# Kernel tuning notes

Measured on AMD Instinct MI355X. Metric: run time of the kernel, lower is better.

Reference implementation:

```python
import jax, jax.numpy as jnp
import numpy as np

B, N, H, W, C = 512, 16, 84, 84, 3
CNN_OUT, ATTN, GH, HEADS, POS, A_DIM = 256, 64, 128, 2, 3, 3
IN_GAT = CNN_OUT + POS  # 259
FLAT = 64 * 16 * 16     # conv output flat dim for 84x84 input


def setup_inputs() -> dict:
    key = jax.random.key(0)
    ks = jax.random.split(key, 16)
    s = 0.05
    return dict(
        cam=jax.random.uniform(ks[0], (B, H, W, C), jnp.float32),
        pos=jax.random.normal(ks[1], (B, POS), jnp.float32),
        team_pos=jax.random.normal(ks[2], (B, N, POS), jnp.float32) * 10.0,
        agent_idx=jax.random.randint(ks[3], (B,), 0, N),
        W1=jax.random.normal(ks[4], (32, C, 8, 8), jnp.float32) * s, b1=jnp.zeros((32,), jnp.float32),
        W2=jax.random.normal(ks[5], (64, 32, 4, 4), jnp.float32) * s, b2=jnp.zeros((64,), jnp.float32),
        W3=jax.random.normal(ks[6], (64, 64, 3, 3), jnp.float32) * s, b3=jnp.zeros((64,), jnp.float32),
        Wp=jax.random.normal(ks[7], (FLAT, CNN_OUT), jnp.float32) * 0.01, bp=jnp.zeros((CNN_OUT,), jnp.float32),
        Wid=jax.random.normal(ks[8], (1, ATTN), jnp.float32) * s, bid=jnp.zeros((ATTN,), jnp.float32),
        Wg=jax.random.normal(ks[9], (IN_GAT, HEADS * GH), jnp.float32) * s,
        a_src=jax.random.normal(ks[10], (HEADS, GH), jnp.float32) * s,
        a_dst=jax.random.normal(ks[11], (HEADS, GH), jnp.float32) * s,
        Wh1=jax.random.normal(ks[12], (HEADS * GH + ATTN, 256), jnp.float32) * s, bh1=jnp.zeros((256,), jnp.float32),
        Wh2=jax.random.normal(ks[13], (256, 2 * A_DIM), jnp.float32) * s, bh2=jnp.zeros((2 * A_DIM,), jnp.float32),
    )


def _conv(x, w, b, stride):
    y = jax.lax.conv_general_dilated(x, w, (stride, stride), 'VALID',
                                     dimension_numbers=('NCHW', 'OIHW', 'NCHW'))
    return jax.nn.relu(y + b[None, :, None, None])


def reference(cam, pos, team_pos, agent_idx, W1, b1, W2, b2, W3, b3, Wp, bp,
              Wid, bid, Wg, a_src, a_dst, Wh1, bh1, Wh2, bh2):
    # CNN encoder (NHWC -> NCHW)
    x = jnp.transpose(cam, (0, 3, 1, 2))
    x = _conv(x, W1, b1, 2)   # [B,32,39,39]
    x = _conv(x, W2, b2, 2)   # [B,64,18,18]
    x = _conv(x, W3, b3, 1)   # [B,64,16,16]
    cam_feat = jax.nn.relu(x.reshape(x.shape[0], -1) @ Wp + bp)  # [B,256]

    # per-node features: broadcast ego cam feat + relative team positions
    rel_pos = team_pos - pos[:, None, :]                                     # [B,N,3]
    node_feats = jnp.concatenate(
        [jnp.broadcast_to(cam_feat[:, None, :], (B, N, CNN_OUT)), rel_pos], axis=-1)  # [B,N,259]

    # adjacency: within 100m, no self-loops, self-loop added for isolated nodes
    dist = jnp.linalg.norm(team_pos[:, :, None, :] - team_pos[:, None, :, :], axis=-1)  # [B,N,N]
    eye = jnp.eye(N, dtype=node_feats.dtype)
    adj = (dist < 100.0).astype(node_feats.dtype) * (1.0 - eye)
    need_self = (adj.sum(axis=2) == 0).astype(adj.dtype)                     # [B,N]
    adj = adj + eye[None] * need_self[..., None]

    # dense multi-head GAT layer
    hN = (node_feats @ Wg).reshape(B, N, HEADS, GH)                          # [B,N,H,D]
    src = jnp.einsum('bnhd,hd->bnh', hN, a_src)
    dst = jnp.einsum('bnhd,hd->bnh', hN, a_dst)
    e = jax.nn.leaky_relu(src[:, :, None, :] + dst[:, None, :, :], 0.2)      # [B,i,j,H]
    e = jnp.where(adj[..., None] > 0, e, -1e9)
    alpha = jax.nn.softmax(e, axis=2)
    h = jnp.einsum('bijh,bjhd->bihd', alpha, hN).reshape(B, N, HEADS * GH)   # [B,N,256]
    h = jax.nn.elu(h)
    h = jnp.nan_to_num(h, nan=0.0, posinf=0.0, neginf=0.0)

    # agent-id embedding, fuse, gather own node, policy head
    id_emb = jax.nn.relu(agent_idx.astype(jnp.float32)[:, None] @ Wid + bid)  # [B,64]
    fused = jnp.concatenate([h, jnp.broadcast_to(id_emb[:, None, :], (B, N, ATTN))], axis=-1)  # [B,N,320]
    agent_feat = fused[jnp.arange(B), agent_idx]                             # [B,320]
    z = jax.nn.relu(agent_feat @ Wh1 + bh1)
    logits = z @ Wh2 + bh2                                                    # [B,6]
    return logits
```

## Files before the change

kernel.cpp:

```cpp
#include <hip/hip_runtime.h>


typedef __attribute__((ext_vector_type(8))) short bf16x8;
typedef __attribute__((ext_vector_type(4))) float f32x4;

union U4 { uint4 v; unsigned int u[4]; bf16x8 h; };

__device__ __forceinline__ unsigned short f2bf(float x) {
    unsigned int u = __float_as_uint(x);
    return (unsigned short)((u + 0x7FFFu + ((u >> 16) & 1u)) >> 16);
}
__device__ __forceinline__ unsigned int pack2(float lo, float hi) {
    return (unsigned int)f2bf(lo) | ((unsigned int)f2bf(hi) << 16);
}
__device__ __forceinline__ bf16x8 loadA(const unsigned int* __restrict__ W, int k8, int M, int oc) {
    U4 r; r.v = *(const uint4*)(W + (((size_t)k8 * M + oc) << 2));
    return r.h;
}
__device__ __forceinline__ bf16x8 loadB4(const unsigned int* __restrict__ base, size_t idx) {
    U4 r; r.v = *(const uint4*)(base + (idx << 2));
    return r.h;
}
#define MFMA(a, b, c) __builtin_amdgcn_mfma_f32_16x16x32_bf16((a), (b), (c), 0, 0, 0)

__device__ __forceinline__ int xcd_swz(int L, int nwg) {
    int q = nwg >> 3, r = nwg & 7;
    int x = L & 7, i = L >> 3;
    return (x < r ? x * (q + 1) : r * (q + 1) + (x - r) * q) + i;
}

__device__ __forceinline__ void storeK(unsigned int* __restrict__ out,
                                       size_t row, size_t BC, size_t bcol,
                                       int lg, unsigned int u0, unsigned int u1) {
    uint2 v; v.x = u0; v.y = u1;
    *(uint2*)(out + ((row * BC + bcol) << 2) + ((lg & 1) << 1)) = v;
}

__global__ __launch_bounds__(256) void prepack(
    const float* __restrict__ W1, const float* __restrict__ W2,
    const float* __restrict__ W3, const float* __restrict__ Wp,
    const float* __restrict__ Wg, const float* __restrict__ Wh1,
    unsigned int* __restrict__ W1t, unsigned int* __restrict__ W2t,
    unsigned int* __restrict__ W3t, unsigned int* __restrict__ Wpt,
    unsigned int* __restrict__ Wgt, unsigned int* __restrict__ Wh1t)
{
    int i = blockIdx.x * 256 + threadIdx.x;
    if (i < 4096) {
        int j2 = i & 3, oc = (i >> 2) & 31, k8 = i >> 7;
        int kh = k8 >> 2, kwp = k8 & 3;
        float w[2];
        #pragma unroll
        for (int e = 0; e < 2; e++) {
            int jj = 2 * j2 + e;
            int kwlo = jj >> 2, c = jj & 3;
            w[e] = (c == 3) ? 0.f
                 : W1[((oc * 3 + c) * 8 + kh) * 8 + 2 * kwp + kwlo];
        }
        W1t[i] = pack2(w[0], w[1]);
    } else if (i < 20480) {
        int j = i - 4096;
        int j2 = j & 3, oc = (j >> 2) & 63, k8 = j >> 8;
        int tap = k8 >> 2, ic = (k8 & 3) * 8 + 2 * j2;
        int kh = tap >> 2, kw = tap & 3;
        float a = W2[((oc * 32 + ic) * 4 + kh) * 4 + kw];
        float b = W2[((oc * 32 + ic + 1) * 4 + kh) * 4 + kw];
        W2t[j] = pack2(a, b);
    } else if (i < 38912) {
        int j = i - 20480;
        int j2 = j & 3, oc = (j >> 2) & 63, k8 = j >> 8;
        int tap = k8 >> 3, ic = (k8 & 7) * 8 + 2 * j2;
        int kh = tap / 3, kw = tap % 3;
        float a = W3[((oc * 64 + ic) * 3 + kh) * 3 + kw];
        float b = W3[((oc * 64 + ic + 1) * 3 + kh) * 3 + kw];
        W3t[j] = pack2(a, b);
    } else if (i < 2136064) {
        int j = i - 38912;
        int j2 = j & 3, n = (j >> 2) & 255, k8 = j >> 10;
        int s3 = k8 >> 3, oc = (k8 & 7) * 8 + 2 * j2;
        float a = Wp[(size_t)(oc * 256 + s3) * 256 + n];
        float b = Wp[(size_t)((oc + 1) * 256 + s3) * 256 + n];
        Wpt[j] = pack2(a, b);
    } else if (i < 2168832) {
        int j = i - 2136064;
        int j2 = j & 3, m = (j >> 2) & 255, k8 = j >> 10;
        int k = k8 * 8 + 2 * j2;
        Wgt[j] = pack2(Wg[k * 256 + m], Wg[(k + 1) * 256 + m]);
    } else if (i < 2209792) {
        int j = i - 2168832;
        int j2 = j & 3, m = (j >> 2) & 255, k8 = j >> 10;
        int k = k8 * 8 + 2 * j2;
        Wh1t[j] = pack2(Wh1[k * 256 + m], Wh1[(k + 1) * 256 + m]);
    }
}

__global__ __launch_bounds__(256) void transpose_cam(
    const float* __restrict__ cam, unsigned int* __restrict__ camq, int b0, int BC)
{
    __shared__ float lds[32][253];
    int yy = blockIdx.x;
    int bb = blockIdx.y * 32;
    int t = threadIdx.x;
    for (int f = t; f < 8064; f += 256) {
        int b = f / 252, p = f - b * 252;
        lds[b][p] = cam[(size_t)(b0 + bb + b) * 21168 + yy * 252 + p];
    }
    __syncthreads();
    for (int g = t; g < 1344; g += 256) {
        int b = g & 31, xp = g >> 5;
        const float* l = &lds[b][6 * xp];
        uint4 u;
        u.x = pack2(l[0], l[1]);
        u.y = pack2(l[2], 0.f);
        u.z = pack2(l[3], l[4]);
        u.w = pack2(l[5], 0.f);
        *(uint4*)(camq + (((size_t)(yy * 42 + xp) * BC + bb + b) << 2)) = u;
    }
}

__global__ __launch_bounds__(256) void conv1_mfma(
    const unsigned int* __restrict__ in32, const unsigned int* __restrict__ Wt,
    const float* __restrict__ bias, unsigned int* __restrict__ out32,
    int BC, int nspat)
{
    int wgid = xcd_swz(blockIdx.x, gridDim.x);
    int s = wgid % nspat;
    int bq = wgid / nspat;
    int oh = s / 39, ow = s - oh * 39;
    int wv = threadIdx.x >> 6, l = threadIdx.x & 63;
    int lg = l >> 4, lc = l & 15;
    const size_t sBC = (size_t)BC;
    size_t base = (size_t)bq * 256 + wv * 64 + lc;
    f32x4 acc[2][4] = {};
    #pragma unroll
    for (int step = 0; step < 8; step++) {
        bf16x8 A[2], B[4];
        A[0] = loadA(Wt, step * 4 + lg, 32, lc);
        A[1] = loadA(Wt, step * 4 + lg, 32, 16 + lc);
        size_t row = (size_t)((2 * oh + step) * 42 + ow + lg);
        #pragma unroll
        for (int g = 0; g < 4; g++)
            B[g] = loadB4(in32, row * sBC + base + g * 16);
        #pragma unroll
        for (int m = 0; m < 2; m++)
            #pragma unroll
            for (int g = 0; g < 4; g++)
                acc[m][g] = MFMA(A[m], B[g], acc[m][g]);
    }
    #pragma unroll
    for (int m = 0; m < 2; m++) {
        float4 bv = *(const float4*)(bias + m * 16 + lg * 4);
        size_t row = (size_t)s * 4 + 2 * m + (lg >> 1);
        #pragma unroll
        for (int g = 0; g < 4; g++) {
            f32x4 a = acc[m][g];
            unsigned int u0 = pack2(fmaxf(a.x + bv.x, 0.f), fmaxf(a.y + bv.y, 0.f));
            unsigned int u1 = pack2(fmaxf(a.z + bv.z, 0.f), fmaxf(a.w + bv.w, 0.f));
            storeK(out32, row, sBC, base + g * 16, lg, u0, u1);
        }
    }
}

__global__ __launch_bounds__(256) void conv2_mfma(
    const unsigned int* __restrict__ in32, const unsigned int* __restrict__ Wt,
    const float* __restrict__ bias, unsigned int* __restrict__ out32,
    int BC, int nspat)
{
    int wgid = xcd_swz(blockIdx.x, gridDim.x);
    int s = wgid % nspat;
    int bq = wgid / nspat;
    int oh = s / 18, ow = s - oh * 18;
    int wv = threadIdx.x >> 6, l = threadIdx.x & 63;
    int lg = l >> 4, lc = l & 15;
    const size_t sBC = (size_t)BC;
    size_t base = (size_t)bq * 256 + wv * 64 + lc;
    f32x4 acc[4][4] = {};
    int ybase = 2 * oh, xbase = 2 * ow;
    #pragma unroll
    for (int sp = 0; sp < 8; sp++) {
        const int s0 = 2 * sp, s1 = s0 + 1;
        bf16x8 A0[4], A1[4], B0[4], B1[4];
        #pragma unroll
        for (int m = 0; m < 4; m++) {
            A0[m] = loadA(Wt, s0 * 4 + lg, 64, m * 16 + lc);
            A1[m] = loadA(Wt, s1 * 4 + lg, 64, m * 16 + lc);
        }
        {
            const int kh = s0 >> 2, kw = s0 & 3;
            size_t row = (size_t)(((ybase + kh) * 39 + xbase + kw) * 4 + lg);
            #pragma unroll
            for (int g = 0; g < 4; g++)
                B0[g] = loadB4(in32, row * sBC + base + g * 16);
        }
        {
            const int kh = s1 >> 2, kw = s1 & 3;
            size_t row = (size_t)(((ybase + kh) * 39 + xbase + kw) * 4 + lg);
            #pragma unroll
            for (int g = 0; g < 4; g++)
                B1[g] = loadB4(in32, row * sBC + base + g * 16);
        }
        #pragma unroll
        for (int m = 0; m < 4; m++)
            #pragma unroll
            for (int g = 0; g < 4; g++)
                acc[m][g] = MFMA(A0[m], B0[g], acc[m][g]);
        #pragma unroll
        for (int m = 0; m < 4; m++)
            #pragma unroll
            for (int g = 0; g < 4; g++)
                acc[m][g] = MFMA(A1[m], B1[g], acc[m][g]);
    }
    #pragma unroll
    for (int m = 0; m < 4; m++) {
        float4 bv = *(const float4*)(bias + m * 16 + lg * 4);
        size_t row = (size_t)s * 8 + 2 * m + (lg >> 1);
        #pragma unroll
        for (int g = 0; g < 4; g++) {
            f32x4 a = acc[m][g];
            unsigned int u0 = pack2(fmaxf(a.x + bv.x, 0.f), fmaxf(a.y + bv.y, 0.f));
            unsigned int u1 = pack2(fmaxf(a.z + bv.z, 0.f), fmaxf(a.w + bv.w, 0.f));
            storeK(out32, row, sBC, base + g * 16, lg, u0, u1);
        }
    }
}

__global__ __launch_bounds__(256) void conv3_mfma(
    const unsigned int* __restrict__ in32, const unsigned int* __restrict__ Wt,
    const float* __restrict__ bias, unsigned int* __restrict__ out32,
    int BC, int nspat)
{
    int wgid = xcd_swz(blockIdx.x, gridDim.x);
    int s = wgid % nspat;
    int bq = wgid / nspat;
    int oh = s >> 4, ow = s & 15;
    int wv = threadIdx.x >> 6, l = threadIdx.x & 63;
    int lg = l >> 4, lc = l & 15;
    const size_t sBC = (size_t)BC;
    size_t base = (size_t)bq * 256 + wv * 64 + lc;
    f32x4 acc[4][4] = {};
    #pragma unroll
    for (int sp = 0; sp < 9; sp++) {
        const int s0 = 2 * sp, s1 = s0 + 1;
        const int kh = sp / 3, kw = sp - kh * 3;
        bf16x8 A0[4], A1[4], B0[4], B1[4];
        #pragma unroll
        for (int m = 0; m < 4; m++) {
            A0[m] = loadA(Wt, s0 * 4 + lg, 64, m * 16 + lc);
            A1[m] = loadA(Wt, s1 * 4 + lg, 64, m * 16 + lc);
        }
        size_t row0 = (size_t)(((oh + kh) * 18 + ow + kw) * 8 + lg);
        #pragma unroll
        for (int g = 0; g < 4; g++) {
            B0[g] = loadB4(in32, row0 * sBC + base + g * 16);
            B1[g] = loadB4(in32, (row0 + 4) * sBC + base + g * 16);
        }
        #pragma unroll
        for (int m = 0; m < 4; m++)
            #pragma unroll
            for (int g = 0; g < 4; g++)
                acc[m][g] = MFMA(A0[m], B0[g], acc[m][g]);
        #pragma unroll
        for (int m = 0; m < 4; m++)
            #pragma unroll
            for (int g = 0; g < 4; g++)
                acc[m][g] = MFMA(A1[m], B1[g], acc[m][g]);
    }
    #pragma unroll
    for (int m = 0; m < 4; m++) {
        float4 bv = *(const float4*)(bias + m * 16 + lg * 4);
        size_t row = (size_t)s * 8 + 2 * m + (lg >> 1);
        #pragma unroll
        for (int g = 0; g < 4; g++) {
            f32x4 a = acc[m][g];
            unsigned int u0 = pack2(fmaxf(a.x + bv.x, 0.f), fmaxf(a.y + bv.y, 0.f));
            unsigned int u1 = pack2(fmaxf(a.z + bv.z, 0.f), fmaxf(a.w + bv.w, 0.f));
            storeK(out32, row, sBC, base + g * 16, lg, u0, u1);
        }
    }
}

__global__ __launch_bounds__(256) void proj_mfma(
    const unsigned int* __restrict__ x3, const unsigned int* __restrict__ Wpt,
    float* __restrict__ partial, int BC)
{
    int wgid = xcd_swz(blockIdx.x, gridDim.x);
    int rem = wgid & 127;
    int bq = wgid >> 7;
    int mq = rem & 3;
    int kseg = rem >> 2;
    int wv = threadIdx.x >> 6, l = threadIdx.x & 63;
    int lg = l >> 4, lc = l & 15;
    const size_t sBC = (size_t)BC;
    size_t base = (size_t)bq * 256 + wv * 64 + lc;
    f32x4 acc[4][4] = {};
    #pragma unroll
    for (int sp = 0; sp < 8; sp++) {
        const int k8b = kseg * 64 + sp * 8;
        bf16x8 A0[4], A1[4], B0[4], B1[4];
        #pragma unroll
        for (int m = 0; m < 4; m++) {
            A0[m] = loadA(Wpt, k8b + lg, 256, mq * 64 + m * 16 + lc);
            A1[m] = loadA(Wpt, k8b + 4 + lg, 256, mq * 64 + m * 16 + lc);
        }
        #pragma unroll
        for (int g = 0; g < 4; g++) {
            B0[g] = loadB4(x3, (size_t)(k8b + lg) * sBC + base + g * 16);
            B1[g] = loadB4(x3, (size_t)(k8b + 4 + lg) * sBC + base + g * 16);
        }
        #pragma unroll
        for (int m = 0; m < 4; m++)
            #pragma unroll
            for (int g = 0; g < 4; g++)
                acc[m][g] = MFMA(A0[m], B0[g], acc[m][g]);
        #pragma unroll
        for (int m = 0; m < 4; m++)
            #pragma unroll
            for (int g = 0; g < 4; g++)
                acc[m][g] = MFMA(A1[m], B1[g], acc[m][g]);
    }
    #pragma unroll
    for (int m = 0; m < 4; m++) {
        size_t row4 = (size_t)kseg * 64 + mq * 16 + m * 4 + lg;
        #pragma unroll
        for (int g = 0; g < 4; g++)
            *(f32x4*)(partial + ((row4 * sBC + base + g * 16) << 2)) = acc[m][g];
    }
}

__global__ __launch_bounds__(256) void reduce_k(
    const float* __restrict__ partial, const float* __restrict__ bp,
    unsigned int* __restrict__ cf16, int b0, int BC, int bcShift)
{
    int i = blockIdx.x * 256 + threadIdx.x;
    int bl = i & (BC - 1);
    int k8 = i >> bcShift;
    f32x4 S0 = {}, S1 = {};
    for (int seg = 0; seg < 32; seg++) {
        const float* p = partial + (((size_t)(seg * 64 + k8 * 2) * BC + bl) << 2);
        S0 += *(const f32x4*)p;
        S1 += *(const f32x4*)(p + (BC << 2));
    }
    int n = k8 * 8;
    uint4 u;
    u.x = pack2(fmaxf(S0.x + bp[n + 0], 0.f), fmaxf(S0.y + bp[n + 1], 0.f));
    u.y = pack2(fmaxf(S0.z + bp[n + 2], 0.f), fmaxf(S0.w + bp[n + 3], 0.f));
    u.z = pack2(fmaxf(S1.x + bp[n + 4], 0.f), fmaxf(S1.y + bp[n + 5], 0.f));
    u.w = pack2(fmaxf(S1.z + bp[n + 6], 0.f), fmaxf(S1.w + bp[n + 7], 0.f));
    *(uint4*)(cf16 + (((size_t)k8 * 512 + b0 + bl) << 2)) = u;
}

__global__ __launch_bounds__(64) void gat_prep(
    const unsigned int* __restrict__ cf16, const unsigned int* __restrict__ Wgt,
    float* __restrict__ hNb)
{
    int mq = blockIdx.x, bq = blockIdx.y;
    int l = threadIdx.x, lg = l >> 4, lc = l & 15;
    size_t bcol = (size_t)bq * 32 + lc;
    f32x4 acc[4][2] = {};
    #pragma unroll
    for (int sp = 0; sp < 4; sp++) {
        const int s0 = 2 * sp, s1 = s0 + 1;
        bf16x8 A0[4], A1[4], B0[2], B1[2];
        #pragma unroll
        for (int m = 0; m < 4; m++) {
            A0[m] = loadA(Wgt, s0 * 4 + lg, 256, mq * 64 + m * 16 + lc);
            A1[m] = loadA(Wgt, s1 * 4 + lg, 256, mq * 64 + m * 16 + lc);
        }
        #pragma unroll
        for (int g = 0; g < 2; g++) {
            B0[g] = loadB4(cf16, (size_t)(s0 * 4 + lg) * 512 + bcol + g * 16);
            B1[g] = loadB4(cf16, (size_t)(s1 * 4 + lg) * 512 + bcol + g * 16);
        }
        #pragma unroll
        for (int m = 0; m < 4; m++) {
            acc[m][0] = MFMA(A0[m], B0[0], acc[m][0]);
            acc[m][1] = MFMA(A0[m], B0[1], acc[m][1]);
            acc[m][0] = MFMA(A1[m], B1[0], acc[m][0]);
            acc[m][1] = MFMA(A1[m], B1[1], acc[m][1]);
        }
    }
    #pragma unroll
    for (int m = 0; m < 4; m++) {
        #pragma unroll
        for (int g = 0; g < 2; g++) {
            size_t b = (size_t)bq * 32 + g * 16 + lc;
            int row0 = mq * 64 + m * 16 + lg * 4;
            *(f32x4*)(hNb + b * 256 + row0) = acc[m][g];
        }
    }
}

__global__ __launch_bounds__(256) void gat_mid(
    const float* __restrict__ hNb, const float* __restrict__ pos,
    const float* __restrict__ tpos, const int* __restrict__ aidx,
    const float* __restrict__ Wg, const float* __restrict__ asrc, const float* __restrict__ adst,
    const float* __restrict__ Wid, const float* __restrict__ bid,
    unsigned int* __restrict__ af16)
{
    int b = blockIdx.x, t = threadIdx.x;
    __shared__ float hN[16][256];
    __shared__ float srcv[16][2], dstv[16][2];
    __shared__ float alpha[16][2];
    __shared__ float af[320];
    __shared__ unsigned int adjm_s;

    int ai = aidx[b];
    float basev = hNb[(size_t)b * 256 + t];
    float rw0 = Wg[65536 + t], rw1 = Wg[65792 + t], rw2 = Wg[66048 + t];
    float px = pos[b * 3 + 0], py = pos[b * 3 + 1], pz = pos[b * 3 + 2];
    for (int n = 0; n < 16; n++) {
        float r0 = tpos[(b * 16 + n) * 3 + 0] - px;
        float r1 = tpos[(b * 16 + n) * 3 + 1] - py;
        float r2 = tpos[(b * 16 + n) * 3 + 2] - pz;
        hN[n][t] = basev + r0 * rw0 + r1 * rw1 + r2 * rw2;
    }

    if (t < 64) {
        bool on = false;
        if (t < 16 && t != ai) {
            float dx = tpos[(b * 16 + ai) * 3 + 0] - tpos[(b * 16 + t) * 3 + 0];
            float dy = tpos[(b * 16 + ai) * 3 + 1] - tpos[(b * 16 + t) * 3 + 1];
            float dz = tpos[(b * 16 + ai) * 3 + 2] - tpos[(b * 16 + t) * 3 + 2];
            on = (dx * dx + dy * dy + dz * dz) < 10000.0f;
        }
        unsigned long long m = __ballot(on);
        if (t == 0) adjm_s = (m == 0ull) ? (1u << ai) : (unsigned int)m;
    }
    __syncthreads();

    {
        int p = t >> 3, sub = t & 7;
        int j = p >> 1, h = p & 1;
        float s1 = 0.f, s2 = 0.f;
        #pragma unroll
        for (int dd = 0; dd < 16; dd++) {
            int d = h * 128 + sub * 16 + dd;
            float v = hN[j][d];
            s1 += v * asrc[d];
            s2 += v * adst[d];
        }
        s1 += __shfl_xor(s1, 1); s1 += __shfl_xor(s1, 2); s1 += __shfl_xor(s1, 4);
        s2 += __shfl_xor(s2, 1); s2 += __shfl_xor(s2, 2); s2 += __shfl_xor(s2, 4);
        if (sub == 0) { srcv[j][h] = s1; dstv[j][h] = s2; }
    }
    __syncthreads();

    if (t < 32) {
        int j = t & 15, h = t >> 4;
        unsigned int am = adjm_s;
        float e = srcv[ai][h] + dstv[j][h];
        e = (e > 0.f) ? e : 0.2f * e;
        e = ((am >> j) & 1u) ? e : -1e9f;
        float mx = e;
        mx = fmaxf(mx, __shfl_xor(mx, 1));
        mx = fmaxf(mx, __shfl_xor(mx, 2));
        mx = fmaxf(mx, __shfl_xor(mx, 4));
        mx = fmaxf(mx, __shfl_xor(mx, 8));
        float ex = __expf(e - mx);
        float sm = ex;
        sm += __shfl_xor(sm, 1); sm += __shfl_xor(sm, 2);
        sm += __shfl_xor(sm, 4); sm += __shfl_xor(sm, 8);
        alpha[j][h] = ex / sm;
    }
    __syncthreads();

    {
        int h = t >> 7;
        float o = 0.f;
        #pragma unroll
        for (int j = 0; j < 16; j++) o += alpha[j][h] * hN[j][t];
        o = (o > 0.f) ? o : (__expf(o) - 1.f);
        af[t] = o;
    }
    if (t < 64) {
        float v = (float)ai * Wid[t] + bid[t];
        af[256 + t] = fmaxf(v, 0.f);
    }
    __syncthreads();

    if (t < 40) {
        uint4 u;
        u.x = pack2(af[t * 8 + 0], af[t * 8 + 1]);
        u.y = pack2(af[t * 8 + 2], af[t * 8 + 3]);
        u.z = pack2(af[t * 8 + 4], af[t * 8 + 5]);
        u.w = pack2(af[t * 8 + 6], af[t * 8 + 7]);
        *(uint4*)(af16 + (((size_t)t * 512 + b) << 2)) = u;
    }
}

__global__ __launch_bounds__(64) void head_mfma(
    const unsigned int* __restrict__ af16, const unsigned int* __restrict__ Wh1t,
    const float* __restrict__ bh1, float* __restrict__ zf)
{
    int mq = blockIdx.x, bq = blockIdx.y;
    int l = threadIdx.x, lg = l >> 4, lc = l & 15;
    size_t bcol = (size_t)bq * 32 + lc;
    f32x4 acc[4][2] = {};
    #pragma unroll
    for (int sp = 0; sp < 5; sp++) {
        const int s0 = 2 * sp, s1 = s0 + 1;
        bf16x8 A0[4], A1[4], B0[2], B1[2];
        #pragma unroll
        for (int m = 0; m < 4; m++) {
            A0[m] = loadA(Wh1t, s0 * 4 + lg, 256, mq * 64 + m * 16 + lc);
            A1[m] = loadA(Wh1t, s1 * 4 + lg, 256, mq * 64 + m * 16 + lc);
        }
        #pragma unroll
        for (int g = 0; g < 2; g++) {
            B0[g] = loadB4(af16, (size_t)(s0 * 4 + lg) * 512 + bcol + g * 16);
            B1[g] = loadB4(af16, (size_t)(s1 * 4 + lg) * 512 + bcol + g * 16);
        }
        #pragma unroll
        for (int m = 0; m < 4; m++) {
            acc[m][0] = MFMA(A0[m], B0[0], acc[m][0]);
            acc[m][1] = MFMA(A0[m], B0[1], acc[m][1]);
            acc[m][0] = MFMA(A1[m], B1[0], acc[m][0]);
            acc[m][1] = MFMA(A1[m], B1[1], acc[m][1]);
        }
    }
    #pragma unroll
    for (int m = 0; m < 4; m++) {
        int row0 = mq * 64 + m * 16 + lg * 4;
        float4 bv = *(const float4*)(bh1 + row0);
        #pragma unroll
        for (int g = 0; g < 2; g++) {
            f32x4 a = acc[m][g];
            size_t b = (size_t)bq * 32 + g * 16 + lc;
            float* pp = zf + (size_t)row0 * 512 + b;
            pp[0]       = fmaxf(a.x + bv.x, 0.f);
            pp[512]     = fmaxf(a.y + bv.y, 0.f);
            pp[2 * 512] = fmaxf(a.z + bv.z, 0.f);
            pp[3 * 512] = fmaxf(a.w + bv.w, 0.f);
        }
    }
}

__global__ __launch_bounds__(256) void logits_k(
    const float* __restrict__ zf, const float* __restrict__ Wh2,
    const float* __restrict__ bh2, float* __restrict__ out)
{
    __shared__ float Ws[1536];
    int t = threadIdx.x;
    int b = blockIdx.x * 256 + t;
    for (int f = t; f < 1536; f += 256) Ws[f] = Wh2[f];
    __syncthreads();
    float acc[6];
    #pragma unroll
    for (int j = 0; j < 6; j++) acc[j] = bh2[j];
    for (int k = 0; k < 256; k++) {
        float zv = zf[(size_t)k * 512 + b];
        #pragma unroll
        for (int j = 0; j < 6; j++) acc[j] += zv * Ws[k * 6 + j];
    }
    #pragma unroll
    for (int j = 0; j < 6; j++) out[b * 6 + j] = acc[j];
}

extern "C" void kernel_launch(void* const* d_in, const int* in_sizes, int n_in,
                              void* d_out, int out_size, void* d_ws, size_t ws_size,
                              hipStream_t stream)
{
    const float* cam  = (const float*)d_in[0];
    const float* pos  = (const float*)d_in[1];
    const float* tpos = (const float*)d_in[2];
    const int*   aidx = (const int*)d_in[3];
    const float* W1   = (const float*)d_in[4];
    const float* b1   = (const float*)d_in[5];
    const float* W2   = (const float*)d_in[6];
    const float* b2   = (const float*)d_in[7];
    const float* W3   = (const float*)d_in[8];
    const float* b3   = (const float*)d_in[9];
    const float* Wp   = (const float*)d_in[10];
    const float* bp   = (const float*)d_in[11];
    const float* Wid  = (const float*)d_in[12];
    const float* bid  = (const float*)d_in[13];
    const float* Wg   = (const float*)d_in[14];
    const float* asrc = (const float*)d_in[15];
    const float* adst = (const float*)d_in[16];
    const float* Wh1  = (const float*)d_in[17];
    const float* bh1  = (const float*)d_in[18];
    const float* Wh2  = (const float*)d_in[19];
    const float* bh2  = (const float*)d_in[20];
    float* out = (float*)d_out;

    int BC = 256;
    if (((size_t)54832 * 512 + 2619392) * 4 <= ws_size) BC = 512;
    int bcShift = (BC == 512) ? 9 : 8;
    int nbq2 = BC >> 8;

    unsigned int* ws32 = (unsigned int*)d_ws;
    unsigned int* RA  = ws32;
    unsigned int* RB  = RA + (size_t)14112 * BC;
    unsigned int* RC  = RB + (size_t)24336 * BC;
    float*        RD  = (float*)(RC + (size_t)8192 * BC);
    unsigned int* W1t = (unsigned int*)(RD + (size_t)8192 * BC);
    unsigned int* W2t  = W1t + 4096;
    unsigned int* W3t  = W2t + 16384;
    unsigned int* Wpt  = W3t + 18432;
    unsigned int* Wgt  = Wpt + 2097152;
    unsigned int* Wh1t = Wgt + 32768;
    unsigned int* cf16 = Wh1t + 40960;
    float*        hNb  = (float*)(cf16 + 65536);
    unsigned int* af16 = (unsigned int*)(hNb + 131072);
    float*        zf   = (float*)(af16 + 81920);

    prepack<<<8632, 256, 0, stream>>>(W1, W2, W3, Wp, Wg, Wh1,
                                      W1t, W2t, W3t, Wpt, Wgt, Wh1t);

    for (int b0 = 0; b0 < 512; b0 += BC) {
        transpose_cam<<<dim3(84, BC / 32), 256, 0, stream>>>(cam, RA, b0, BC);
        conv1_mfma<<<1521 * nbq2, 256, 0, stream>>>(RA, W1t, b1, RB, BC, 1521);
        conv2_mfma<<<324 * nbq2, 256, 0, stream>>>(RB, W2t, b2, RA, BC, 324);
        conv3_mfma<<<256 * nbq2, 256, 0, stream>>>(RA, W3t, b3, RC, BC, 256);
        proj_mfma<<<128 * nbq2, 256, 0, stream>>>(RC, Wpt, RD, BC);
        reduce_k<<<(32 * BC) / 256, 256, 0, stream>>>(RD, bp, cf16, b0, BC, bcShift);
    }
    gat_prep<<<dim3(4, 16), 64, 0, stream>>>(cf16, Wgt, hNb);
    gat_mid<<<512, 256, 0, stream>>>(hNb, pos, tpos, aidx, Wg, asrc, adst,
                                     Wid, bid, af16);
    head_mfma<<<dim3(4, 16), 64, 0, stream>>>(af16, Wh1t, bh1, zf);
    logits_k<<<2, 256, 0, stream>>>(zf, Wh2, bh2, out);
}
```

Baseline: 149.3 us.

## Compute two conv1 output rows per block and narrow proj batch tile

```diff
diff --git a/kernel.cpp b/kernel.cpp
--- a/kernel.cpp
+++ b/kernel.cpp
@@ -117,7 +117,7 @@
     }
 }
 
-__global__ __launch_bounds__(256) void conv1_mfma(
+__global__ __launch_bounds__(256) void conv1_pair(
     const unsigned int* __restrict__ in32, const unsigned int* __restrict__ Wt,
     const float* __restrict__ bias, unsigned int* __restrict__ out32,
     int BC, int nspat)
@@ -125,37 +125,64 @@
     int wgid = xcd_swz(blockIdx.x, gridDim.x);
     int s = wgid % nspat;
     int bq = wgid / nspat;
-    int oh = s / 39, ow = s - oh * 39;
+    int ohp = s / 39, ow = s - ohp * 39;
+    int oh0 = 2 * ohp;
+    const bool has2 = (oh0 + 1) < 39;
     int wv = threadIdx.x >> 6, l = threadIdx.x & 63;
     int lg = l >> 4, lc = l & 15;
     const size_t sBC = (size_t)BC;
     size_t base = (size_t)bq * 256 + wv * 64 + lc;
-    f32x4 acc[2][4] = {};
-    #pragma unroll
-    for (int step = 0; step < 8; step++) {
-        bf16x8 A[2], B[4];
-        A[0] = loadA(Wt, step * 4 + lg, 32, lc);
-        A[1] = loadA(Wt, step * 4 + lg, 32, 16 + lc);
-        size_t row = (size_t)((2 * oh + step) * 42 + ow + lg);
-        #pragma unroll
-        for (int g = 0; g < 4; g++)
-            B[g] = loadB4(in32, row * sBC + base + g * 16);
-        #pragma unroll
-        for (int m = 0; m < 2; m++)
+    f32x4 acc0[2][4] = {}, acc1[2][4] = {};
+    bf16x8 Ar0[2], Ar1[2];
+    #pragma unroll
+    for (int t = 0; t < 10; t++) {
+        const int par = t & 1;
+        bf16x8 B[4];
+        if (t < 8 || has2) {
+            size_t row = (size_t)((2 * oh0 + t) * 42 + ow + lg);
             #pragma unroll
             for (int g = 0; g < 4; g++)
-                acc[m][g] = MFMA(A[m], B[g], acc[m][g]);
-    }
+                B[g] = loadB4(in32, row * sBC + base + g * 16);
+        }
+        if (t >= 2 && has2) {
+            #pragma unroll
+            for (int g = 0; g < 4; g++) {
+                acc1[0][g] = MFMA(Ar0[par], B[g], acc1[0][g]);
+                acc1[1][g] = MFMA(Ar1[par], B[g], acc1[1][g]);
+            }
+        }
+        if (t < 8) {
+            bf16x8 An0 = loadA(Wt, t * 4 + lg, 32, lc);
+            bf16x8 An1 = loadA(Wt, t * 4 + lg, 32, 16 + lc);
+            #pragma unroll
+            for (int g = 0; g < 4; g++) {
+                acc0[0][g] = MFMA(An0, B[g], acc0[0][g]);
+                acc0[1][g] = MFMA(An1, B[g], acc0[1][g]);
+            }
+            Ar0[par] = An0; Ar1[par] = An1;
+        }
+    }
+    int s0 = oh0 * 39 + ow;
     #pragma unroll
     for (int m = 0; m < 2; m++) {
         float4 bv = *(const float4*)(bias + m * 16 + lg * 4);
-        size_t row = (size_t)s * 4 + 2 * m + (lg >> 1);
+        size_t row = (size_t)s0 * 4 + 2 * m + (lg >> 1);
         #pragma unroll
         for (int g = 0; g < 4; g++) {
-            f32x4 a = acc[m][g];
+            f32x4 a = acc0[m][g];
             unsigned int u0 = pack2(fmaxf(a.x + bv.x, 0.f), fmaxf(a.y + bv.y, 0.f));
             unsigned int u1 = pack2(fmaxf(a.z + bv.z, 0.f), fmaxf(a.w + bv.w, 0.f));
             storeK(out32, row, sBC, base + g * 16, lg, u0, u1);
+        }
+        if (has2) {
+            size_t row1 = row + 4 * 39;
+            #pragma unroll
+            for (int g = 0; g < 4; g++) {
+                f32x4 a = acc1[m][g];
+                unsigned int u0 = pack2(fmaxf(a.x + bv.x, 0.f), fmaxf(a.y + bv.y, 0.f));
+                unsigned int u1 = pack2(fmaxf(a.z + bv.z, 0.f), fmaxf(a.w + bv.w, 0.f));
+                storeK(out32, row1, sBC, base + g * 16, lg, u0, u1);
+            }
         }
     }
 }
@@ -284,44 +311,44 @@
 {
     int wgid = xcd_swz(blockIdx.x, gridDim.x);
     int rem = wgid & 127;
-    int bq = wgid >> 7;
+    int b128 = wgid >> 7;
     int mq = rem & 3;
     int kseg = rem >> 2;
     int wv = threadIdx.x >> 6, l = threadIdx.x & 63;
     int lg = l >> 4, lc = l & 15;
     const size_t sBC = (size_t)BC;
-    size_t base = (size_t)bq * 256 + wv * 64 + lc;
-    f32x4 acc[4][4] = {};
+    size_t base = (size_t)b128 * 128 + wv * 32 + lc;
+    f32x4 acc[4][2] = {};
     #pragma unroll
     for (int sp = 0; sp < 8; sp++) {
         const int k8b = kseg * 64 + sp * 8;
-        bf16x8 A0[4], A1[4], B0[4], B1[4];
+        bf16x8 A0[4], A1[4], B0[2], B1[2];
         #pragma unroll
         for (int m = 0; m < 4; m++) {
             A0[m] = loadA(Wpt, k8b + lg, 256, mq * 64 + m * 16 + lc);
             A1[m] = loadA(Wpt, k8b + 4 + lg, 256, mq * 64 + m * 16 + lc);
         }
         #pragma unroll
-        for (int g = 0; g < 4; g++) {
+        for (int g = 0; g < 2; g++) {
             B0[g] = loadB4(x3, (size_t)(k8b + lg) * sBC + base + g * 16);
             B1[g] = loadB4(x3, (size_t)(k8b + 4 + lg) * sBC + base + g * 16);
         }
         #pragma unroll
         for (int m = 0; m < 4; m++)
             #pragma unroll
-            for (int g = 0; g < 4; g++)
+            for (int g = 0; g < 2; g++)
                 acc[m][g] = MFMA(A0[m], B0[g], acc[m][g]);
         #pragma unroll
         for (int m = 0; m < 4; m++)
             #pragma unroll
-            for (int g = 0; g < 4; g++)
+            for (int g = 0; g < 2; g++)
                 acc[m][g] = MFMA(A1[m], B1[g], acc[m][g]);
     }
     #pragma unroll
     for (int m = 0; m < 4; m++) {
         size_t row4 = (size_t)kseg * 64 + mq * 16 + m * 4 + lg;
         #pragma unroll
-        for (int g = 0; g < 4; g++)
+        for (int g = 0; g < 2; g++)
             *(f32x4*)(partial + ((row4 * sBC + base + g * 16) << 2)) = acc[m][g];
     }
 }
@@ -608,10 +635,10 @@
 
     for (int b0 = 0; b0 < 512; b0 += BC) {
         transpose_cam<<<dim3(84, BC / 32), 256, 0, stream>>>(cam, RA, b0, BC);
-        conv1_mfma<<<1521 * nbq2, 256, 0, stream>>>(RA, W1t, b1, RB, BC, 1521);
+        conv1_pair<<<780 * nbq2, 256, 0, stream>>>(RA, W1t, b1, RB, BC, 780);
         conv2_mfma<<<324 * nbq2, 256, 0, stream>>>(RB, W2t, b2, RA, BC, 324);
         conv3_mfma<<<256 * nbq2, 256, 0, stream>>>(RA, W3t, b3, RC, BC, 256);
-        proj_mfma<<<128 * nbq2, 256, 0, stream>>>(RC, Wpt, RD, BC);
+        proj_mfma<<<128 * (BC >> 7), 256, 0, stream>>>(RC, Wpt, RD, BC);
         reduce_k<<<(32 * BC) / 256, 256, 0, stream>>>(RD, bp, cf16, b0, BC, bcShift);
     }
     gat_prep<<<dim3(4, 16), 64, 0, stream>>>(cf16, Wgt, hNb);
```

New measurement: 151.1 us. Within noise of the previous version (+1.2%).
